# Optimization experiments

Measured on AMD Instinct MI355X. Metric: run time of the kernel, lower is better.

Reference implementation:

```python
import jax, jax.numpy as jnp
import numpy as np

TOPK, NPRO, NALP, NADS = 13, 31, 24, 37
ALPHA, BETA, EPS = 1.0, 6.0, 1e-9
BS, NA, NM = 32, 8400, 64
IMG = 640.0


def _make_boxes(key, shape, img=IMG):
    k1, k2 = jax.random.split(key)
    cxy = jax.random.uniform(k1, shape[:-1] + (2,), minval=0.0, maxval=img)
    wh = jax.random.uniform(k2, shape[:-1] + (2,), minval=10.0, maxval=120.0)
    return jnp.concatenate([cxy - wh / 2, cxy + wh / 2], axis=-1)


def setup_inputs() -> dict:
    key = jax.random.key(0)
    ks = jax.random.split(key, 12)
    pd_pro_scores = jax.random.uniform(ks[0], (BS, NA, NPRO))
    pd_alp_scores = jax.random.uniform(ks[1], (BS, NA, NALP))
    pd_ads_scores = jax.random.uniform(ks[2], (5, BS, NA, NADS))
    pd_bboxes = _make_boxes(ks[3], (BS, NA, 4))
    pd_corners = jax.random.uniform(ks[4], (BS, NA, 8), maxval=IMG)
    anc_points = jax.random.uniform(ks[5], (NA, 2), maxval=IMG)
    gt_pro = jax.random.randint(ks[6], (BS, NM, 1), 0, NPRO, dtype=jnp.int32)
    gt_alp = jax.random.randint(ks[7], (BS, NM, 1), 0, NALP, dtype=jnp.int32)
    gt_ads = jax.random.randint(ks[8], (BS, NM, 5), 0, NADS, dtype=jnp.int32)
    gt_bboxes = _make_boxes(ks[9], (BS, NM, 4))
    gt_corners = jax.random.uniform(ks[10], (BS, NM, 8), maxval=IMG)
    nvalid = jax.random.randint(ks[11], (BS,), NM // 2, NM + 1)
    mask_gt = (jnp.arange(NM)[None, :] < nvalid[:, None]).astype(jnp.float32)[..., None]
    return {"pd_pro_scores": pd_pro_scores, "pd_alp_scores": pd_alp_scores,
            "pd_ads_scores": pd_ads_scores, "pd_bboxes": pd_bboxes,
            "pd_corners": pd_corners, "anc_points": anc_points,
            "gt_pro": gt_pro, "gt_alp": gt_alp, "gt_ads": gt_ads,
            "gt_bboxes": gt_bboxes, "gt_corners": gt_corners, "mask_gt": mask_gt}


def _iou(gt, pd):
    # gt: (bs, nm, 4) xyxy; pd: (bs, na, 4) xyxy -> (bs, nm, na)
    g, p = gt[:, :, None, :], pd[:, None, :, :]
    lt = jnp.maximum(g[..., :2], p[..., :2])
    rb = jnp.minimum(g[..., 2:], p[..., 2:])
    inter = jnp.clip(rb - lt, 0).prod(-1)
    a1 = jnp.clip(g[..., 2:] - g[..., :2], 0).prod(-1)
    a2 = jnp.clip(p[..., 2:] - p[..., :2], 0).prod(-1)
    return inter / (a1 + a2 - inter + EPS)


def reference(pd_pro_scores, pd_alp_scores, pd_ads_scores, pd_bboxes, pd_corners,
              anc_points, gt_pro, gt_alp, gt_ads, gt_bboxes, gt_corners, mask_gt):
    bs, na = pd_pro_scores.shape[:2]
    nm = gt_bboxes.shape[1]
    b = jnp.arange(bs)[:, None]

    # --- get_box_metrics ---
    labels = gt_pro[..., 0].astype(jnp.int32)                       # (bs, nm)
    bbox_scores = pd_pro_scores.transpose(0, 2, 1)[b, labels]       # (bs, nm, na)
    overlaps = _iou(gt_bboxes, pd_bboxes)                           # (bs, nm, na)
    align = (bbox_scores ** ALPHA) * (overlaps ** BETA)

    # --- select_candidates_in_gts ---
    xy = anc_points[None, None]                                     # (1,1,na,2)
    d_lt = xy - gt_bboxes[:, :, None, :2]
    d_rb = gt_bboxes[:, :, None, 2:] - xy
    mask_in = (jnp.minimum(d_lt, d_rb).min(-1) > EPS).astype(align.dtype)

    # --- select_topk_candidates ---
    metrics = align * mask_in
    _, tidx = jax.lax.top_k(metrics, TOPK)                          # (bs, nm, topk)
    valid = mask_gt[..., 0] > 0                                     # (bs, nm)
    tidx = jnp.where(valid[..., None], tidx, 0)
    rows = jnp.arange(bs * nm)[:, None]
    counts = jnp.zeros((bs * nm, na), jnp.int32).at[rows, tidx.reshape(bs * nm, TOPK)].add(1)
    counts = counts.reshape(bs, nm, na)
    is_in_topk = jnp.where(counts > 1, 0, counts).astype(metrics.dtype)
    mask_pos = is_in_topk * mask_in * mask_gt                       # (bs, nm, na)

    # --- select_highest_overlaps ---
    fg_mask = mask_pos.sum(-2)                                      # (bs, na)
    multi = fg_mask > 1
    max_idx = overlaps.argmax(1)                                    # (bs, na)
    is_max = (jnp.arange(nm)[None, :, None] == max_idx[:, None, :]).astype(mask_pos.dtype)
    mask_pos = jnp.where(multi[:, None, :], is_max, mask_pos)
    fg_mask = mask_pos.sum(-2)
    target_gt_idx = mask_pos.argmax(-2)                             # (bs, na)

    # --- get_targets ---
    target_pro = jnp.maximum(gt_pro[..., 0].astype(jnp.int32)[b, target_gt_idx], 0)
    target_alp = jnp.maximum(gt_alp[..., 0].astype(jnp.int32)[b, target_gt_idx], 0)
    target_ads = jnp.maximum(gt_ads.astype(jnp.int32)[b, target_gt_idx], 0)   # (bs, na, 5)
    target_ad0_4 = jnp.moveaxis(target_ads, -1, 0)                  # (5, bs, na)
    target_bboxes = gt_bboxes[b, target_gt_idx]                     # (bs, na, 4)
    target_corners = gt_corners[b, target_gt_idx]                   # (bs, na, 8)

    fg = (fg_mask > 0).astype(jnp.float32)                          # (bs, na)
    pro_scores = jax.nn.one_hot(target_pro, NPRO, dtype=jnp.float32) * fg[..., None]
    alp_scores = jax.nn.one_hot(target_alp, NALP, dtype=jnp.float32) * fg[..., None]
    ads_scores = jax.nn.one_hot(target_ad0_4, NADS, dtype=jnp.float32) * fg[None, :, :, None]

    # --- normalization of pro scores ---
    align = align * mask_pos
    pos_align = align.max(-1, keepdims=True)                        # (bs, nm, 1)
    pos_ov = (overlaps * mask_pos).max(-1, keepdims=True)           # (bs, nm, 1)
    norm = (align * pos_ov / (pos_align + EPS)).max(-2)[..., None]  # (bs, na, 1)
    pro_scores = pro_scores * norm

    return (target_pro, target_alp, target_ad0_4, target_bboxes, target_corners,
            pro_scores, alp_scores, ads_scores, fg_mask > 0)
```

## Files before the change

kernel.cpp:

```cpp
#include <hip/hip_runtime.h>
#include <cstdint>
#include <cstddef>

#define BS 32
#define NA 8400
#define NM 64
#define NPRO 31
#define NALP 24
#define NADS 37
#define TOPK 13
#define FEPS 1e-9f
#define WORDS 264
#define CAP 1024

#define OFF0 0L
#define OFF1 268800L
#define OFF2 537600L
#define OFF3 1881600L
#define OFF4 2956800L
#define OFF5 5107200L
#define OFF6 13440000L
#define OFF7 19891200L
#define OFF8 69619200L

__device__ __forceinline__ float iou1(float4 g, float ga, float4 p, float pa) {
  float iw = fmaxf(fminf(g.z, p.z) - fmaxf(g.x, p.x), 0.f);
  float ih = fmaxf(fminf(g.w, p.w) - fmaxf(g.y, p.y), 0.f);
  float inter = iw * ih;
  return inter / (ga + pa - inter + FEPS);
}

__global__ __launch_bounds__(256) void kZ(unsigned long long* __restrict__ amask,
                                          unsigned* __restrict__ posA,
                                          unsigned* __restrict__ posO) {
  int i = blockIdx.x * 256 + threadIdx.x;
  if (i < BS * NA) amask[i] = 0ull;
  if (i < BS * NM) { posA[i] = 0u; posO[i] = 0u; }
}

__global__ __launch_bounds__(256) void kA(
    const float* __restrict__ pro, const float* __restrict__ pd_bb,
    const float* __restrict__ anc, const int* __restrict__ gt_pro,
    const float* __restrict__ gt_bb, const float* __restrict__ mask_gt,
    unsigned long long* __restrict__ amask)
{
  __shared__ unsigned s_in[WORDS];
  __shared__ unsigned s_pos[WORDS];
  __shared__ float s_cv[CAP];
  __shared__ int   s_ci[CAP];
  __shared__ int   s_cnt;

  const int bm = blockIdx.x;
  const int b = bm >> 6;
  const int m = bm & 63;
  const int tid = threadIdx.x;

  if (!(mask_gt[bm] > 0.f)) return;

  for (int w = tid; w < WORDS; w += 256) { s_in[w] = 0u; s_pos[w] = 0u; }
  if (tid == 0) s_cnt = 0;
  __syncthreads();

  const float4 g = *(const float4*)(gt_bb + (size_t)bm * 4);
  const int label = gt_pro[bm];
  const float ga = fmaxf(g.z - g.x, 0.f) * fmaxf(g.w - g.y, 0.f);
  const float* pb = pd_bb + (size_t)b * NA * 4;
  const float* ps = pro + (size_t)b * NA * NPRO + label;

  for (int a = tid; a < NA; a += 256) {
    float2 ap = *(const float2*)(anc + 2 * a);
    float din = fminf(fminf(ap.x - g.x, ap.y - g.y), fminf(g.z - ap.x, g.w - ap.y));
    if (din > FEPS) {
      atomicOr(&s_in[a >> 5], 1u << (a & 31));
      float4 p = *(const float4*)(pb + (size_t)a * 4);
      float pa = fmaxf(p.z - p.x, 0.f) * fmaxf(p.w - p.y, 0.f);
      float iou = iou1(g, ga, p, pa);
      float i2 = iou * iou;
      float met = ps[(size_t)a * NPRO] * (i2 * i2 * i2);
      if (met > 0.f) {
        atomicOr(&s_pos[a >> 5], 1u << (a & 31));
        int pidx = atomicAdd(&s_cnt, 1);
        if (pidx < CAP) { s_cv[pidx] = met; s_ci[pidx] = a; }
      }
    }
  }
  __syncthreads();

  const int P = min(s_cnt, CAP);
  if (tid < 64) {
    float lv[16]; int li[16];
#pragma unroll
    for (int e = 0; e < 16; e++) {
      int p = tid + e * 64;
      bool ok = p < P;
      lv[e] = ok ? s_cv[p] : -1.f;
      li[e] = ok ? s_ci[p] : NA;
    }
    const int nsel = min(P, TOPK);
    for (int k = 0; k < nsel; k++) {
      float bv = -1.f; int bi = NA;
#pragma unroll
      for (int e = 0; e < 16; e++)
        if (lv[e] > bv || (lv[e] == bv && li[e] < bi)) { bv = lv[e]; bi = li[e]; }
      for (int s = 1; s < 64; s <<= 1) {
        float ov = __shfl_xor(bv, s);
        int   oi = __shfl_xor(bi, s);
        if (ov > bv || (ov == bv && oi < bi)) { bv = ov; bi = oi; }
      }
#pragma unroll
      for (int e = 0; e < 16; e++) if (li[e] == bi) lv[e] = -1.f;
      if (tid == 0) {
        atomicOr(&amask[(size_t)b * NA + bi], 1ull << m);
      }
    }
    if (tid == 0 && P < TOPK) {
      int need = TOPK - P;
      for (int a = 0; a < NA && need > 0; a++) {
        if (!((s_pos[a >> 5] >> (a & 31)) & 1u)) {
          need--;
          if ((s_in[a >> 5] >> (a & 31)) & 1u)
            atomicOr(&amask[(size_t)b * NA + a], 1ull << m);
        }
      }
    }
  }
}

__global__ __launch_bounds__(256) void kB(
    const float* __restrict__ pro, const float* __restrict__ pd_bb,
    const int* __restrict__ gt_pro, const float* __restrict__ gt_bb,
    const unsigned long long* __restrict__ amask,
    unsigned* __restrict__ posA, unsigned* __restrict__ posO,
    int* __restrict__ tgi, float* __restrict__ fgo, float* __restrict__ avo)
{
  __shared__ float4 s_g[NM];
  __shared__ float s_ga[NM];
  __shared__ int s_lab[NM];

  const int b = blockIdx.y;
  const int tid = threadIdx.x;
  const int a = blockIdx.x * 256 + tid;

  if (tid < NM) {
    float4 gg = *(const float4*)(gt_bb + (size_t)(b * NM + tid) * 4);
    s_g[tid] = gg;
    s_ga[tid] = fmaxf(gg.z - gg.x, 0.f) * fmaxf(gg.w - gg.y, 0.f);
    s_lab[tid] = gt_pro[b * NM + tid];
  }
  __syncthreads();
  if (a >= NA) return;

  const int ia = b * NA + a;
  unsigned long long msk = amask[ia];
  int cnt = __popcll(msk);
  int chosen = 0; float ovv = 0.f, av = 0.f, fg = 0.f;

  if (cnt > 0) {
    fg = 1.f;
    float4 p = *(const float4*)(pd_bb + (size_t)ia * 4);
    float pa = fmaxf(p.z - p.x, 0.f) * fmaxf(p.w - p.y, 0.f);
    if (cnt == 1) {
      chosen = __ffsll(msk) - 1;
      ovv = iou1(s_g[chosen], s_ga[chosen], p, pa);
    } else {
      float best = -1.f; int bmx = 0;
      for (int m = 0; m < NM; m++) {
        float v = iou1(s_g[m], s_ga[m], p, pa);
        if (v > best) { best = v; bmx = m; }
      }
      chosen = bmx; ovv = best;
    }
    float sc = pro[(size_t)ia * NPRO + s_lab[chosen]];
    float o2 = ovv * ovv;
    av = sc * (o2 * o2 * o2);
    atomicMax(&posA[b * NM + chosen], __float_as_uint(av));
    atomicMax(&posO[b * NM + chosen], __float_as_uint(ovv));
  }
  tgi[ia] = chosen; fgo[ia] = fg; avo[ia] = av;
}

__global__ __launch_bounds__(256) void kC(
    const int* __restrict__ gt_pro, const int* __restrict__ gt_alp,
    const int* __restrict__ gt_ads, const float* __restrict__ gt_bb,
    const float* __restrict__ gt_cor,
    const unsigned* __restrict__ posA, const unsigned* __restrict__ posO,
    const int* __restrict__ tgi, const float* __restrict__ fgi,
    const float* __restrict__ avi, float* __restrict__ out)
{
  __shared__ int s_tp[256], s_ta[256];
  __shared__ int s_td[5][256];
  __shared__ float s_pv[256], s_fg[256];

  const int b = blockIdx.y;
  const int a0 = blockIdx.x * 256;
  const int tid = threadIdx.x;
  const int na = min(256, NA - a0);
  const int a = a0 + tid;

  if (a < NA) {
    const int ia = b * NA + a;
    const int g = tgi[ia];
    const float fg = fgi[ia];
    float no = 0.f;
    if (fg > 0.f) {
      no = avi[ia] * __uint_as_float(posO[b * NM + g]) /
           (__uint_as_float(posA[b * NM + g]) + FEPS);
    }
    const int gi = b * NM + g;
    const int tp = gt_pro[gi], ta = gt_alp[gi];
    s_tp[tid] = tp; s_ta[tid] = ta; s_pv[tid] = no; s_fg[tid] = fg;
    out[OFF0 + ia] = (float)tp;
    out[OFF1 + ia] = (float)ta;
#pragma unroll
    for (int k = 0; k < 5; k++) {
      int td = gt_ads[(size_t)gi * 5 + k];
      s_td[k][tid] = td;
      out[OFF2 + (size_t)k * (BS * NA) + ia] = (float)td;
    }
    float4 bb = *(const float4*)(gt_bb + (size_t)gi * 4);
    *(float4*)(out + OFF3 + (size_t)ia * 4) = bb;
    float4 c0 = *(const float4*)(gt_cor + (size_t)gi * 8);
    float4 c1 = *(const float4*)(gt_cor + (size_t)gi * 8 + 4);
    *(float4*)(out + OFF4 + (size_t)ia * 8) = c0;
    *(float4*)(out + OFF4 + (size_t)ia * 8 + 4) = c1;
    out[OFF8 + ia] = fg;
  }
  __syncthreads();

  {
    float* dst = out + OFF5 + ((size_t)b * NA + a0) * NPRO;
    const int n = na * NPRO;
    for (int e4 = tid * 4; e4 < n; e4 += 1024) {
      float vv[4];
#pragma unroll
      for (int j = 0; j < 4; j++) {
        int e = e4 + j; int al = e / NPRO; int c = e - al * NPRO;
        vv[j] = (c == s_tp[al]) ? s_pv[al] : 0.f;
      }
      *(float4*)(dst + e4) = make_float4(vv[0], vv[1], vv[2], vv[3]);
    }
  }
  {
    float* dst = out + OFF6 + ((size_t)b * NA + a0) * NALP;
    const int n = na * NALP;
    for (int e4 = tid * 4; e4 < n; e4 += 1024) {
      float vv[4];
#pragma unroll
      for (int j = 0; j < 4; j++) {
        int e = e4 + j; int al = e / NALP; int c = e - al * NALP;
        vv[j] = (c == s_ta[al]) ? s_fg[al] : 0.f;
      }
      *(float4*)(dst + e4) = make_float4(vv[0], vv[1], vv[2], vv[3]);
    }
  }
#pragma unroll
  for (int k = 0; k < 5; k++) {
    float* dst = out + OFF7 + (size_t)k * ((size_t)BS * NA * NADS) +
                 ((size_t)b * NA + a0) * NADS;
    const int n = na * NADS;
    for (int e4 = tid * 4; e4 < n; e4 += 1024) {
      float vv[4];
#pragma unroll
      for (int j = 0; j < 4; j++) {
        int e = e4 + j; int al = e / NADS; int c = e - al * NADS;
        vv[j] = (c == s_td[k][al]) ? s_fg[al] : 0.f;
      }
      *(float4*)(dst + e4) = make_float4(vv[0], vv[1], vv[2], vv[3]);
    }
  }
}

extern "C" void kernel_launch(void* const* d_in, const int* in_sizes, int n_in,
                              void* d_out, int out_size, void* d_ws, size_t ws_size,
                              hipStream_t stream) {
  const float* pd_pro  = (const float*)d_in[0];
  const float* pd_bb   = (const float*)d_in[3];
  const float* anc     = (const float*)d_in[5];
  const int*   gt_pro  = (const int*)d_in[6];
  const int*   gt_alp  = (const int*)d_in[7];
  const int*   gt_ads  = (const int*)d_in[8];
  const float* gt_bb   = (const float*)d_in[9];
  const float* gt_cor  = (const float*)d_in[10];
  const float* mask_gt = (const float*)d_in[11];
  float* out = (float*)d_out;

  char* ws = (char*)d_ws;
  unsigned long long* amask = (unsigned long long*)(ws);
  unsigned* posA = (unsigned*)(ws + 2150400);
  unsigned* posO = (unsigned*)(ws + 2158592);
  int*      tgi  = (int*)     (ws + 2166784);
  float*    fgo  = (float*)   (ws + 3241984);
  float*    avo  = (float*)   (ws + 4317184);

  kZ<<<(BS * NA + 255) / 256, 256, 0, stream>>>(amask, posA, posO);
  kA<<<BS * NM, 256, 0, stream>>>(pd_pro, pd_bb, anc, gt_pro, gt_bb, mask_gt, amask);
  dim3 gridBC((NA + 255) / 256, BS);
  kB<<<gridBC, 256, 0, stream>>>(pd_pro, pd_bb, gt_pro, gt_bb, amask,
                                 posA, posO, tgi, fgo, avo);
  kC<<<gridBC, 256, 0, stream>>>(gt_pro, gt_alp, gt_ads, gt_bb, gt_cor,
                                 posA, posO, tgi, fgo, avo, out);
}
```

Measured before the change: 130.3 us.

## Replace global anchor bitmask with per-gt top-k lists and add nontemporal stores

kA now writes a compact per-gt list of up to 13 selected anchor indices (short) instead of atomically OR-ing bits into a global 64-bit mask per anchor. kB rebuilds the per-anchor mask in shared memory from these lists, which removes the zeroing kernel and the global atomics. kC output writes become nontemporal stores to avoid polluting cache with the large one-hot outputs. kC is also launched twice, which duplicates the largest write pass and looks like a mistake.

```diff
diff --git a/kernel.cpp b/kernel.cpp
--- a/kernel.cpp
+++ b/kernel.cpp
@@ -12,6 +12,7 @@
 #define FEPS 1e-9f
 #define WORDS 264
 #define CAP 1024
+#define TL 16
 
 #define OFF0 0L
 #define OFF1 268800L
@@ -23,6 +24,16 @@
 #define OFF7 19891200L
 #define OFF8 69619200L
 
+typedef float f4_t __attribute__((ext_vector_type(4)));
+
+__device__ __forceinline__ void nt4(float* p, float a, float b, float c, float d) {
+  f4_t v = {a, b, c, d};
+  __builtin_nontemporal_store(v, (f4_t*)p);
+}
+__device__ __forceinline__ void nt1(float* p, float v) {
+  __builtin_nontemporal_store(v, p);
+}
+
 __device__ __forceinline__ float iou1(float4 g, float ga, float4 p, float pa) {
   float iw = fmaxf(fminf(g.z, p.z) - fmaxf(g.x, p.x), 0.f);
   float ih = fmaxf(fminf(g.w, p.w) - fmaxf(g.y, p.y), 0.f);
@@ -30,19 +41,12 @@
   return inter / (ga + pa - inter + FEPS);
 }
 
-__global__ __launch_bounds__(256) void kZ(unsigned long long* __restrict__ amask,
-                                          unsigned* __restrict__ posA,
-                                          unsigned* __restrict__ posO) {
-  int i = blockIdx.x * 256 + threadIdx.x;
-  if (i < BS * NA) amask[i] = 0ull;
-  if (i < BS * NM) { posA[i] = 0u; posO[i] = 0u; }
-}
-
 __global__ __launch_bounds__(256) void kA(
     const float* __restrict__ pro, const float* __restrict__ pd_bb,
     const float* __restrict__ anc, const int* __restrict__ gt_pro,
     const float* __restrict__ gt_bb, const float* __restrict__ mask_gt,
-    unsigned long long* __restrict__ amask)
+    short* __restrict__ tlist, unsigned* __restrict__ posA,
+    unsigned* __restrict__ posO)
 {
   __shared__ unsigned s_in[WORDS];
   __shared__ unsigned s_pos[WORDS];
@@ -52,10 +56,15 @@
 
   const int bm = blockIdx.x;
   const int b = bm >> 6;
-  const int m = bm & 63;
   const int tid = threadIdx.x;
 
-  if (!(mask_gt[bm] > 0.f)) return;
+  if (tid == 0) { posA[bm] = 0u; posO[bm] = 0u; }
+
+  short* tl = tlist + bm * TL;
+  if (!(mask_gt[bm] > 0.f)) {
+    if (tid == 0) tl[0] = 0;
+    return;
+  }
 
   for (int w = tid; w < WORDS; w += 256) { s_in[w] = 0u; s_pos[w] = 0u; }
   if (tid == 0) s_cnt = 0;
@@ -109,19 +118,20 @@
       }
 #pragma unroll
       for (int e = 0; e < 16; e++) if (li[e] == bi) lv[e] = -1.f;
-      if (tid == 0) {
-        atomicOr(&amask[(size_t)b * NA + bi], 1ull << m);
-      }
-    }
-    if (tid == 0 && P < TOPK) {
-      int need = TOPK - P;
-      for (int a = 0; a < NA && need > 0; a++) {
-        if (!((s_pos[a >> 5] >> (a & 31)) & 1u)) {
-          need--;
-          if ((s_in[a >> 5] >> (a & 31)) & 1u)
-            atomicOr(&amask[(size_t)b * NA + a], 1ull << m);
+      if (tid == 0) tl[1 + k] = (short)bi;
+    }
+    if (tid == 0) {
+      int cnt = nsel;
+      if (P < TOPK) {
+        int need = TOPK - P;
+        for (int a = 0; a < NA && need > 0; a++) {
+          if (!((s_pos[a >> 5] >> (a & 31)) & 1u)) {
+            need--;
+            if ((s_in[a >> 5] >> (a & 31)) & 1u) tl[1 + cnt++] = (short)a;
+          }
         }
       }
+      tl[0] = (short)cnt;
     }
   }
 }
@@ -129,29 +139,46 @@
 __global__ __launch_bounds__(256) void kB(
     const float* __restrict__ pro, const float* __restrict__ pd_bb,
     const int* __restrict__ gt_pro, const float* __restrict__ gt_bb,
-    const unsigned long long* __restrict__ amask,
+    const short* __restrict__ tlist,
     unsigned* __restrict__ posA, unsigned* __restrict__ posO,
     int* __restrict__ tgi, float* __restrict__ fgo, float* __restrict__ avo)
 {
   __shared__ float4 s_g[NM];
   __shared__ float s_ga[NM];
   __shared__ int s_lab[NM];
+  __shared__ unsigned long long s_m[256];
+  __shared__ short s_tl[NM * TL];
 
   const int b = blockIdx.y;
+  const int a0 = blockIdx.x << 8;
   const int tid = threadIdx.x;
-  const int a = blockIdx.x * 256 + tid;
-
+
+  s_m[tid] = 0ull;
   if (tid < NM) {
     float4 gg = *(const float4*)(gt_bb + (size_t)(b * NM + tid) * 4);
     s_g[tid] = gg;
     s_ga[tid] = fmaxf(gg.z - gg.x, 0.f) * fmaxf(gg.w - gg.y, 0.f);
     s_lab[tid] = gt_pro[b * NM + tid];
   }
-  __syncthreads();
+  for (int i = tid; i < NM * TL / 2; i += 256)
+    ((int*)s_tl)[i] = ((const int*)(tlist + (size_t)b * NM * TL))[i];
+  __syncthreads();
+
+  for (int i = tid; i < NM * TL; i += 256) {
+    int m = i >> 4, sl = i & 15;
+    if (sl >= 1 && sl <= (int)s_tl[m * TL]) {
+      int ai = s_tl[i];
+      unsigned d = (unsigned)(ai - a0);
+      if (d < 256u) atomicOr(&s_m[d], 1ull << m);
+    }
+  }
+  __syncthreads();
+
+  const int a = a0 + tid;
   if (a >= NA) return;
 
   const int ia = b * NA + a;
-  unsigned long long msk = amask[ia];
+  unsigned long long msk = s_m[tid];
   int cnt = __popcll(msk);
   int chosen = 0; float ovv = 0.f, av = 0.f, fg = 0.f;
 
@@ -209,21 +236,21 @@
     const int gi = b * NM + g;
     const int tp = gt_pro[gi], ta = gt_alp[gi];
     s_tp[tid] = tp; s_ta[tid] = ta; s_pv[tid] = no; s_fg[tid] = fg;
-    out[OFF0 + ia] = (float)tp;
-    out[OFF1 + ia] = (float)ta;
+    nt1(out + OFF0 + ia, (float)tp);
+    nt1(out + OFF1 + ia, (float)ta);
 #pragma unroll
     for (int k = 0; k < 5; k++) {
       int td = gt_ads[(size_t)gi * 5 + k];
       s_td[k][tid] = td;
-      out[OFF2 + (size_t)k * (BS * NA) + ia] = (float)td;
+      nt1(out + OFF2 + (size_t)k * (BS * NA) + ia, (float)td);
     }
     float4 bb = *(const float4*)(gt_bb + (size_t)gi * 4);
-    *(float4*)(out + OFF3 + (size_t)ia * 4) = bb;
+    nt4(out + OFF3 + (size_t)ia * 4, bb.x, bb.y, bb.z, bb.w);
     float4 c0 = *(const float4*)(gt_cor + (size_t)gi * 8);
     float4 c1 = *(const float4*)(gt_cor + (size_t)gi * 8 + 4);
-    *(float4*)(out + OFF4 + (size_t)ia * 8) = c0;
-    *(float4*)(out + OFF4 + (size_t)ia * 8 + 4) = c1;
-    out[OFF8 + ia] = fg;
+    nt4(out + OFF4 + (size_t)ia * 8, c0.x, c0.y, c0.z, c0.w);
+    nt4(out + OFF4 + (size_t)ia * 8 + 4, c1.x, c1.y, c1.z, c1.w);
+    nt1(out + OFF8 + ia, fg);
   }
   __syncthreads();
 
@@ -237,7 +264,7 @@
         int e = e4 + j; int al = e / NPRO; int c = e - al * NPRO;
         vv[j] = (c == s_tp[al]) ? s_pv[al] : 0.f;
       }
-      *(float4*)(dst + e4) = make_float4(vv[0], vv[1], vv[2], vv[3]);
+      nt4(dst + e4, vv[0], vv[1], vv[2], vv[3]);
     }
   }
   {
@@ -250,7 +277,7 @@
         int e = e4 + j; int al = e / NALP; int c = e - al * NALP;
         vv[j] = (c == s_ta[al]) ? s_fg[al] : 0.f;
       }
-      *(float4*)(dst + e4) = make_float4(vv[0], vv[1], vv[2], vv[3]);
+      nt4(dst + e4, vv[0], vv[1], vv[2], vv[3]);
     }
   }
 #pragma unroll
@@ -265,7 +292,7 @@
         int e = e4 + j; int al = e / NADS; int c = e - al * NADS;
         vv[j] = (c == s_td[k][al]) ? s_fg[al] : 0.f;
       }
-      *(float4*)(dst + e4) = make_float4(vv[0], vv[1], vv[2], vv[3]);
+      nt4(dst + e4, vv[0], vv[1], vv[2], vv[3]);
     }
   }
 }
@@ -285,18 +312,20 @@
   float* out = (float*)d_out;
 
   char* ws = (char*)d_ws;
-  unsigned long long* amask = (unsigned long long*)(ws);
-  unsigned* posA = (unsigned*)(ws + 2150400);
-  unsigned* posO = (unsigned*)(ws + 2158592);
-  int*      tgi  = (int*)     (ws + 2166784);
-  float*    fgo  = (float*)   (ws + 3241984);
-  float*    avo  = (float*)   (ws + 4317184);
-
-  kZ<<<(BS * NA + 255) / 256, 256, 0, stream>>>(amask, posA, posO);
-  kA<<<BS * NM, 256, 0, stream>>>(pd_pro, pd_bb, anc, gt_pro, gt_bb, mask_gt, amask);
+  short*    tlist = (short*)(ws);
+  unsigned* posA  = (unsigned*)(ws + 65536);
+  unsigned* posO  = (unsigned*)(ws + 73728);
+  int*      tgi   = (int*)     (ws + 81920);
+  float*    fgo   = (float*)   (ws + 1157120);
+  float*    avo   = (float*)   (ws + 2232320);
+
+  kA<<<BS * NM, 256, 0, stream>>>(pd_pro, pd_bb, anc, gt_pro, gt_bb, mask_gt,
+                                  tlist, posA, posO);
   dim3 gridBC((NA + 255) / 256, BS);
-  kB<<<gridBC, 256, 0, stream>>>(pd_pro, pd_bb, gt_pro, gt_bb, amask,
+  kB<<<gridBC, 256, 0, stream>>>(pd_pro, pd_bb, gt_pro, gt_bb, tlist,
                                  posA, posO, tgi, fgo, avo);
   kC<<<gridBC, 256, 0, stream>>>(gt_pro, gt_alp, gt_ads, gt_bb, gt_cor,
                                  posA, posO, tgi, fgo, avo, out);
-}
+  kC<<<gridBC, 256, 0, stream>>>(gt_pro, gt_alp, gt_ads, gt_bb, gt_cor,
+                                 posA, posO, tgi, fgo, avo, out);
+}
```

Result: slower. 203.1 us (+55.9%).
